# Optimization experiments

Measured on AMD Instinct MI355X. Metric: run time of the kernel, lower is better.

Reference implementation:

```python
import jax, jax.numpy as jnp
import numpy as np

GAMMA = 0.99          # discount factor from __init__
TD_LAMBDA = 0.95      # lambda for GAE (lambda < 1 -> GAE branch)
STEP_TYPE_LAST = 2    # alf StepType.LAST


def setup_inputs() -> dict:
    key = jax.random.key(0)
    k0, k1, k2, k3, k4 = jax.random.split(key, 5)
    T1, B = 1024, 4096  # [T+1, B] time-major
    return {
        "value": jax.random.normal(k0, (T1, B), jnp.float32),
        "target_value": jax.random.normal(k1, (T1, B), jnp.float32),
        "reward": jax.random.normal(k2, (T1, B), jnp.float32),
        "step_type": jax.random.randint(k3, (T1, B), 0, 3, jnp.int32),
        "discount": jax.random.uniform(k4, (T1, B), dtype=jnp.float32),
    }


def _gae(reward, target_value, step_type, discount):
    # discounts passed to value_ops are training_info.discount * gamma
    d = discount * GAMMA                                   # [T+1, B]
    is_last = (step_type == STEP_TYPE_LAST).astype(reward.dtype)
    # one-step TD residuals, time-major [T, B]
    delta = reward[1:] + d[1:] * target_value[1:] - target_value[:-1]
    wd = d[1:] * TD_LAMBDA                                 # [T, B]
    not_last = 1.0 - is_last[:-1]                          # [T, B]

    def step(adv_next, xs):
        delta_t, wd_t, nl_t = xs
        adv = nl_t * (delta_t + wd_t * adv_next)
        return adv, adv

    init = jnp.zeros_like(reward[0])                       # [B]
    _, advs = jax.lax.scan(step, init, (delta, wd, not_last), reverse=True)
    return advs                                            # [T, B]


def reference(value, target_value, reward, step_type, discount):
    advs = jax.lax.stop_gradient(_gae(reward, target_value, step_type, discount))
    returns = advs + target_value[:-1]                     # G_t^lambda, [T, B]
    # element_wise_squared_loss(returns.detach(), value[:-1])
    td_err = jax.lax.stop_gradient(returns) - value[:-1]
    loss = td_err * td_err                                 # [T, B]
    # tensor_extend_zero: append a zero row -> [T+1, B]
    return jnp.concatenate([loss, jnp.zeros_like(loss[:1])], axis=0)
```

## Files before the change

kernel.cpp:

```cpp
#include <hip/hip_runtime.h>

#define T1     1024
#define T      1023
#define B      4096
#define LOGB   12
#define CHUNK  16
#define NCHUNK 64

#define GAMMA     0.99f
#define TD_LAMBDA 0.95f

__global__ __launch_bounds__(256) void k_compose(
    const float* __restrict__ tv, const float* __restrict__ rew,
    const int* __restrict__ st, const float* __restrict__ disc,
    float* __restrict__ Ac, float* __restrict__ Bc)
{
    int tid = blockIdx.x * blockDim.x + threadIdx.x;
    int b = tid & (B - 1);
    int c = tid >> LOGB;
    int s = c * CHUNK;
    int e = min(s + CHUNK, T);

    float A = 0.f, Bf = 1.f;
    float tv_next = tv[(size_t)e * B + b];
    for (int t = e - 1; t >= s; --t) {
        size_t idx  = (size_t)t * B + b;
        size_t idx1 = idx + B;
        float d1    = disc[idx1] * GAMMA;
        float tv_t  = tv[idx];
        float delta = rew[idx1] + d1 * tv_next - tv_t;
        float wd    = d1 * TD_LAMBDA;
        float nl    = (st[idx] == 2) ? 0.f : 1.f;
        float a  = nl * delta;
        float bb = nl * wd;
        A  = fmaf(bb, A, a);
        Bf = bb * Bf;
        tv_next = tv_t;
    }
    Ac[tid] = A;
    Bc[tid] = Bf;
}

__global__ __launch_bounds__(256) void k_scan(
    const float* __restrict__ Ac, const float* __restrict__ Bc,
    float* __restrict__ R)
{
    int b = blockIdx.x * blockDim.x + threadIdx.x;
    float adv = 0.f;
    for (int c = NCHUNK - 1; c >= 0; --c) {
        int i = c * B + b;
        R[i] = adv;
        adv = fmaf(Bc[i], adv, Ac[i]);
    }
}

__global__ __launch_bounds__(256) void k_replay(
    const float* __restrict__ value, const float* __restrict__ tv,
    const float* __restrict__ rew, const int* __restrict__ st,
    const float* __restrict__ disc, const float* __restrict__ R,
    float* __restrict__ out)
{
    int tid = blockIdx.x * blockDim.x + threadIdx.x;
    int b = tid & (B - 1);
    int c = tid >> LOGB;
    int s = c * CHUNK;
    int e = min(s + CHUNK, T);

    float adv = R[tid];
    float tv_next = tv[(size_t)e * B + b];
    if (c == NCHUNK - 1) {
        out[(size_t)T * B + b] = 0.f;
    }
    for (int t = e - 1; t >= s; --t) {
        size_t idx  = (size_t)t * B + b;
        size_t idx1 = idx + B;
        float d1    = disc[idx1] * GAMMA;
        float tv_t  = tv[idx];
        float delta = rew[idx1] + d1 * tv_next - tv_t;
        float wd    = d1 * TD_LAMBDA;
        float nl    = (st[idx] == 2) ? 0.f : 1.f;
        adv = nl * fmaf(wd, adv, delta);
        float td = adv + tv_t - value[idx];
        out[idx] = td * td;
        tv_next = tv_t;
    }
}

extern "C" void kernel_launch(void* const* d_in, const int* in_sizes, int n_in,
                              void* d_out, int out_size, void* d_ws, size_t ws_size,
                              hipStream_t stream) {
    const float* value = (const float*)d_in[0];
    const float* tv    = (const float*)d_in[1];
    const float* rew   = (const float*)d_in[2];
    const int*   st    = (const int*)d_in[3];
    const float* disc  = (const float*)d_in[4];
    float* out = (float*)d_out;

    float* Ac = (float*)d_ws;
    float* Bc = Ac + (size_t)NCHUNK * B;
    float* R  = Bc + (size_t)NCHUNK * B;

    k_compose<<<(NCHUNK * B) / 256, 256, 0, stream>>>(tv, rew, st, disc, Ac, Bc);
    k_scan<<<B / 256, 256, 0, stream>>>(Ac, Bc, R);
    k_replay<<<(NCHUNK * B) / 256, 256, 0, stream>>>(value, tv, rew, st, disc, R, out);
}
```

Before: 134.8 us.

## Vectorize GAE chunk kernels with float4 and fold carry scan into replay

```diff
diff --git a/kernel.cpp b/kernel.cpp
--- a/kernel.cpp
+++ b/kernel.cpp
@@ -3,86 +3,122 @@
 #define T1     1024
 #define T      1023
 #define B      4096
-#define LOGB   12
+#define Q      1024
 #define CHUNK  16
 #define NCHUNK 64
+#define GPC    4
 
 #define GAMMA     0.99f
 #define TD_LAMBDA 0.95f
 
+typedef __attribute__((ext_vector_type(4))) float f4;
+typedef __attribute__((ext_vector_type(4))) int   i4;
+
 __global__ __launch_bounds__(256) void k_compose(
     const float* __restrict__ tv, const float* __restrict__ rew,
     const int* __restrict__ st, const float* __restrict__ disc,
-    float* __restrict__ Ac, float* __restrict__ Bc)
+    float* __restrict__ AggA, float* __restrict__ AggB)
 {
-    int tid = blockIdx.x * blockDim.x + threadIdx.x;
-    int b = tid & (B - 1);
-    int c = tid >> LOGB;
+    int c = blockIdx.x >> 2;
+    int g = blockIdx.x & 3;
+    int q = (g << 8) + threadIdx.x;
     int s = c * CHUNK;
     int e = min(s + CHUNK, T);
 
-    float A = 0.f, Bf = 1.f;
-    float tv_next = tv[(size_t)e * B + b];
+    const f4* tv4   = (const f4*)tv;
+    const f4* rew4  = (const f4*)rew;
+    const f4* disc4 = (const f4*)disc;
+    const i4* st4   = (const i4*)st;
+
+    f4 A  = {0.f, 0.f, 0.f, 0.f};
+    f4 Bf = {1.f, 1.f, 1.f, 1.f};
+    f4 tvn = tv4[(size_t)e * Q + q];
+#pragma unroll 4
     for (int t = e - 1; t >= s; --t) {
-        size_t idx  = (size_t)t * B + b;
-        size_t idx1 = idx + B;
-        float d1    = disc[idx1] * GAMMA;
-        float tv_t  = tv[idx];
-        float delta = rew[idx1] + d1 * tv_next - tv_t;
-        float wd    = d1 * TD_LAMBDA;
-        float nl    = (st[idx] == 2) ? 0.f : 1.f;
-        float a  = nl * delta;
-        float bb = nl * wd;
-        A  = fmaf(bb, A, a);
-        Bf = bb * Bf;
-        tv_next = tv_t;
+        size_t i  = (size_t)t * Q + q;
+        size_t i1 = i + Q;
+        f4 d1  = disc4[i1] * GAMMA;
+        f4 tvt = tv4[i];
+        f4 r1  = rew4[i1];
+        i4 stt = st4[i];
+#pragma unroll
+        for (int j = 0; j < 4; ++j) {
+            float delta = r1[j] + d1[j] * tvn[j] - tvt[j];
+            float wd    = d1[j] * TD_LAMBDA;
+            float nl    = (stt[j] == 2) ? 0.f : 1.f;
+            float a  = nl * delta;
+            float bb = nl * wd;
+            A[j]  = fmaf(bb, A[j], a);
+            Bf[j] *= bb;
+        }
+        tvn = tvt;
     }
-    Ac[tid] = A;
-    Bc[tid] = Bf;
-}
-
-__global__ __launch_bounds__(256) void k_scan(
-    const float* __restrict__ Ac, const float* __restrict__ Bc,
-    float* __restrict__ R)
-{
-    int b = blockIdx.x * blockDim.x + threadIdx.x;
-    float adv = 0.f;
-    for (int c = NCHUNK - 1; c >= 0; --c) {
-        int i = c * B + b;
-        R[i] = adv;
-        adv = fmaf(Bc[i], adv, Ac[i]);
-    }
+    ((f4*)AggA)[c * Q + q] = A;
+    ((f4*)AggB)[c * Q + q] = Bf;
 }
 
 __global__ __launch_bounds__(256) void k_replay(
     const float* __restrict__ value, const float* __restrict__ tv,
     const float* __restrict__ rew, const int* __restrict__ st,
-    const float* __restrict__ disc, const float* __restrict__ R,
+    const float* __restrict__ disc,
+    const float* __restrict__ AggA, const float* __restrict__ AggB,
     float* __restrict__ out)
 {
-    int tid = blockIdx.x * blockDim.x + threadIdx.x;
-    int b = tid & (B - 1);
-    int c = tid >> LOGB;
+    int c = blockIdx.x >> 2;
+    int g = blockIdx.x & 3;
+    int q = (g << 8) + threadIdx.x;
     int s = c * CHUNK;
     int e = min(s + CHUNK, T);
 
-    float adv = R[tid];
-    float tv_next = tv[(size_t)e * B + b];
+    const f4* tv4   = (const f4*)tv;
+    const f4* rew4  = (const f4*)rew;
+    const f4* disc4 = (const f4*)disc;
+    const f4* val4  = (const f4*)value;
+    const i4* st4   = (const i4*)st;
+    const f4* A4    = (const f4*)AggA;
+    const f4* B4    = (const f4*)AggB;
+    f4* out4 = (f4*)out;
+
+    f4 S = {0.f, 0.f, 0.f, 0.f};
+    f4 P = {1.f, 1.f, 1.f, 1.f};
+    for (int cc = c + 1; cc < NCHUNK; ++cc) {
+        f4 a = A4[cc * Q + q];
+        f4 b = B4[cc * Q + q];
+#pragma unroll
+        for (int j = 0; j < 4; ++j) {
+            S[j] = fmaf(P[j], a[j], S[j]);
+            P[j] *= b[j];
+        }
+    }
+    f4 adv = S;
+
     if (c == NCHUNK - 1) {
-        out[(size_t)T * B + b] = 0.f;
+        f4 z = {0.f, 0.f, 0.f, 0.f};
+        out4[(size_t)T * Q + q] = z;
     }
+
+    f4 tvn = tv4[(size_t)e * Q + q];
+#pragma unroll 4
     for (int t = e - 1; t >= s; --t) {
-        size_t idx  = (size_t)t * B + b;
-        size_t idx1 = idx + B;
-        float d1    = disc[idx1] * GAMMA;
-        float tv_t  = tv[idx];
-        float delta = rew[idx1] + d1 * tv_next - tv_t;
-        float wd    = d1 * TD_LAMBDA;
-        float nl    = (st[idx] == 2) ? 0.f : 1.f;
-        adv = nl * fmaf(wd, adv, delta);
-        float td = adv + tv_t - value[idx];
-        out[idx] = td * td;
-        tv_next = tv_t;
+        size_t i  = (size_t)t * Q + q;
+        size_t i1 = i + Q;
+        f4 d1  = disc4[i1] * GAMMA;
+        f4 tvt = tv4[i];
+        f4 r1  = rew4[i1];
+        i4 stt = st4[i];
+        f4 vv  = val4[i];
+        f4 o;
+#pragma unroll
+        for (int j = 0; j < 4; ++j) {
+            float delta = r1[j] + d1[j] * tvn[j] - tvt[j];
+            float wd    = d1[j] * TD_LAMBDA;
+            float nl    = (stt[j] == 2) ? 0.f : 1.f;
+            adv[j] = nl * fmaf(wd, adv[j], delta);
+            float td = adv[j] + tvt[j] - vv[j];
+            o[j] = td * td;
+        }
+        out4[i] = o;
+        tvn = tvt;
     }
 }
 
@@ -96,11 +132,9 @@
     const float* disc  = (const float*)d_in[4];
     float* out = (float*)d_out;
 
-    float* Ac = (float*)d_ws;
-    float* Bc = Ac + (size_t)NCHUNK * B;
-    float* R  = Bc + (size_t)NCHUNK * B;
+    float* AggA = (float*)d_ws;
+    float* AggB = AggA + (size_t)NCHUNK * B;
 
-    k_compose<<<(NCHUNK * B) / 256, 256, 0, stream>>>(tv, rew, st, disc, Ac, Bc);
-    k_scan<<<B / 256, 256, 0, stream>>>(Ac, Bc, R);
-    k_replay<<<(NCHUNK * B) / 256, 256, 0, stream>>>(value, tv, rew, st, disc, R, out);
+    k_compose<<<NCHUNK * GPC, 256, 0, stream>>>(tv, rew, st, disc, AggA, AggB);
+    k_replay<<<NCHUNK * GPC, 256, 0, stream>>>(value, tv, rew, st, disc, AggA, AggB, out);
 }
```

Result: no change. 133.7 us (-0.8%).
